# Kernel tuning notes

Measured on AMD Instinct MI355X. Metric: run time of the kernel, lower is better.

## Reference

```python
import jax, jax.numpy as jnp
import numpy as np

N_NODES = 100000
N_EDGES = 1250000
D_FEAT = 64
UNITS = 64


def setup_inputs() -> dict:
    key = jax.random.key(0)
    k1, k2, k3 = jax.random.split(key, 3)
    features = jax.random.normal(k1, (N_NODES, D_FEAT), dtype=jnp.float32)
    edge_index = jax.random.randint(k2, (2, N_EDGES), 0, N_NODES, dtype=jnp.int64)
    weight = jax.random.normal(k3, (D_FEAT, UNITS), dtype=jnp.float32) * (1.0 / np.sqrt(D_FEAT))
    bias = jnp.zeros((UNITS,), dtype=jnp.float32)
    return {"features": features, "edge_index": edge_index, "weight": weight, "bias": bias}


def reference(features, edge_index, weight, bias):
    num_nodes = features.shape[0]
    row = edge_index[0]  # [E] destination rows of adjacency
    col = edge_index[1]  # [E] source columns
    ones = jnp.ones(row.shape[0], dtype=features.dtype)
    # degree_i = number of edges with row == i (sparse row-sum of all-ones adj)
    degrees = jax.ops.segment_sum(ones, row, num_segments=num_nodes)
    deg_inv_sqrt = jnp.power(degrees, -0.5)
    deg_inv_sqrt = jnp.where(jnp.isfinite(deg_inv_sqrt), deg_inv_sqrt, 0.0)
    # symmetric normalization per edge: D^{-1/2} A D^{-1/2}
    w = deg_inv_sqrt[row] * deg_inv_sqrt[col]  # [E]
    # SpMM: propagated[i] = sum_{e: row_e = i} w_e * features[col_e]
    msgs = features[col] * w[:, None]  # [E, F]
    propagated = jax.ops.segment_sum(msgs, row, num_segments=num_nodes)  # [N, F]
    h = propagated @ weight + bias
    return jax.nn.relu(h)
```

## Files before the change

kernel.cpp:

```cpp
#include <hip/hip_runtime.h>
#include <hip/hip_bf16.h>

#define DFEAT 64
#define SBSHIFT 9
#define SBROWS 512
#define CAPSHIFT 13
#define CAP 8192
#define CHUNK 2048

typedef __attribute__((ext_vector_type(8))) unsigned short ushort8;

static __device__ __forceinline__ unsigned short f2bf(float f) {
    __hip_bfloat16 h = __float2bfloat16(f);
    unsigned short u;
    __builtin_memcpy(&u, &h, 2);
    return u;
}

__global__ __launch_bounds__(256) void xw_binA_kernel(
        const float* __restrict__ feat, const float* __restrict__ W,
        ushort8* __restrict__ Y, int n,
        const int* __restrict__ ei, int E,
        int* __restrict__ sbcursor, int* __restrict__ packed, int xwBlocks) {
    __shared__ float4 sW[DFEAT * 16];
    __shared__ int hist[256];
    __shared__ int cur[256];

    if (blockIdx.x < xwBlocks) {
        for (int i = threadIdx.x; i < DFEAT * 16; i += blockDim.x)
            sW[i] = ((const float4*)W)[i];
        __syncthreads();

        int q = threadIdx.x & 3;
        int lrow = threadIdx.x >> 2;
        int lane = threadIdx.x & 63;
        int qbase = lane & ~3;
        int row = blockIdx.x * 64 + lrow;

        float4 x[4];
        if (row < n) {
            const float4* xp = (const float4*)(feat + (size_t)row * DFEAT) + q * 4;
            x[0] = xp[0]; x[1] = xp[1]; x[2] = xp[2]; x[3] = xp[3];
        } else {
            x[0] = x[1] = x[2] = x[3] = make_float4(0.f, 0.f, 0.f, 0.f);
        }

        float4 acc[4];
#pragma unroll
        for (int j = 0; j < 4; j++) acc[j] = make_float4(0.f, 0.f, 0.f, 0.f);

#pragma unroll
        for (int qp = 0; qp < 4; qp++) {
#pragma unroll
            for (int jj = 0; jj < 4; jj++) {
                float xs[4];
                xs[0] = __shfl(x[jj].x, qbase + qp);
                xs[1] = __shfl(x[jj].y, qbase + qp);
                xs[2] = __shfl(x[jj].z, qbase + qp);
                xs[3] = __shfl(x[jj].w, qbase + qp);
                int k0 = qp * 16 + jj * 4;
#pragma unroll
                for (int c = 0; c < 4; c++) {
                    const float4* wrow = &sW[(k0 + c) * 16 + q * 4];
#pragma unroll
                    for (int j = 0; j < 4; j++) {
                        float4 w = wrow[j];
                        acc[j].x = fmaf(xs[c], w.x, acc[j].x);
                        acc[j].y = fmaf(xs[c], w.y, acc[j].y);
                        acc[j].z = fmaf(xs[c], w.z, acc[j].z);
                        acc[j].w = fmaf(xs[c], w.w, acc[j].w);
                    }
                }
            }
        }

        if (row < n) {
            ushort8 o0, o1;
            o0[0] = f2bf(acc[0].x); o0[1] = f2bf(acc[0].y);
            o0[2] = f2bf(acc[0].z); o0[3] = f2bf(acc[0].w);
            o0[4] = f2bf(acc[1].x); o0[5] = f2bf(acc[1].y);
            o0[6] = f2bf(acc[1].z); o0[7] = f2bf(acc[1].w);
            o1[0] = f2bf(acc[2].x); o1[1] = f2bf(acc[2].y);
            o1[2] = f2bf(acc[2].z); o1[3] = f2bf(acc[2].w);
            o1[4] = f2bf(acc[3].x); o1[5] = f2bf(acc[3].y);
            o1[6] = f2bf(acc[3].z); o1[7] = f2bf(acc[3].w);
            ushort8* Yo = Y + (size_t)row * 8 + q * 2;
            Yo[0] = o0;
            Yo[1] = o1;
        }
    } else {
        int bid = blockIdx.x - xwBlocks;
        int t = threadIdx.x;
        hist[t] = 0;
        __syncthreads();
        int base = bid * CHUNK;
        for (int k = 0; k < CHUNK; k += 256) {
            int idx = base + k + t;
            if (idx < E) atomicAdd(&hist[ei[idx] >> SBSHIFT], 1);
        }
        __syncthreads();
        int h = hist[t];
        cur[t] = (h > 0) ? atomicAdd(&sbcursor[t], h) : 0;
        __syncthreads();
        for (int k = 0; k < CHUNK; k += 256) {
            int idx = base + k + t;
            if (idx < E) {
                int r = ei[idx];
                int c = ei[E + idx];
                int sb = r >> SBSHIFT;
                int p = atomicAdd(&cur[sb], 1);
                if (p < CAP)
                    packed[(sb << CAPSHIFT) + p] = ((r & (SBROWS - 1)) << 17) | c;
            }
        }
    }
}

__global__ void binB_kernel(const int* __restrict__ sbcursor, const int* __restrict__ packed,
                            int* __restrict__ csr_col, int* __restrict__ row_beg,
                            int* __restrict__ row_end, float* __restrict__ dis, int n) {
    __shared__ int rcnt[SBROWS];
    __shared__ int rcur[SBROWS];
    int sb = blockIdx.x;
    int t = threadIdx.x;
    int cnt = min(sbcursor[sb], CAP);
    const int* pk = packed + ((size_t)sb << CAPSHIFT);
    for (int i = t; i < SBROWS; i += 256) rcnt[i] = 0;
    __syncthreads();
    for (int i = t; i < cnt; i += 256) atomicAdd(&rcnt[pk[i] >> 17], 1);
    __syncthreads();
    if (t < 64) {
        int v[8];
        int run = 0;
#pragma unroll
        for (int k = 0; k < 8; k++) { v[k] = run; run += rcnt[t * 8 + k]; }
        int x = run;
        for (int off = 1; off < 64; off <<= 1) {
            int y = __shfl_up(x, off);
            if (t >= off) x += y;
        }
        int excl = x - run;
#pragma unroll
        for (int k = 0; k < 8; k++) rcur[t * 8 + k] = excl + v[k];
    }
    __syncthreads();
    int rows = min(SBROWS, n - sb * SBROWS);
    for (int rl = t; rl < rows; rl += 256) {
        int beg = (sb << CAPSHIFT) + rcur[rl];
        int d = rcnt[rl];
        int r = sb * SBROWS + rl;
        row_beg[r] = beg;
        row_end[r] = beg + d;
        dis[r] = (d > 0) ? rsqrtf((float)d) : 0.0f;
    }
    __syncthreads();
    for (int i = t; i < cnt; i += 256) {
        int p = pk[i];
        int pos = atomicAdd(&rcur[p >> 17], 1);
        csr_col[(sb << CAPSHIFT) + pos] = p & 0x1FFFF;
    }
}

__global__ __launch_bounds__(256) void spmm_kernel(
        const int* __restrict__ row_beg, const int* __restrict__ row_end,
        const int* __restrict__ csr_col, const float* __restrict__ dis,
        const ushort8* __restrict__ Y, const float* __restrict__ bias,
        float* __restrict__ out, int n) {
    int wid = (int)(((long long)blockIdx.x * blockDim.x + threadIdx.x) >> 6);
    int lane = threadIdx.x & 63;
    int h = lane >> 5;
    int lane5 = lane & 31;
    int hbase = h << 5;
    int row = wid * 2 + h;
    bool active = row < n;
    int s = active ? row_beg[row] : 0;
    int e = active ? row_end[row] : 0;
    int sub = lane5 >> 3;
    int f8 = lane5 & 7;
    float acc[8] = {0.f, 0.f, 0.f, 0.f, 0.f, 0.f, 0.f, 0.f};
    for (int base = s; base < e; base += 32) {
        int cnt = min(32, e - base);
        int c = 0;
        float dv = 0.f;
        if (lane5 < cnt) { c = csr_col[base + lane5]; dv = dis[c]; }
        for (int i = 0; i < cnt; i += 4) {
            int idx = i + sub;
            int ce = __shfl(c, hbase + idx);
            float de = __shfl(dv, hbase + idx);
            if (idx < cnt) {
                ushort8 y = Y[(size_t)ce * 8 + f8];
#pragma unroll
                for (int k = 0; k < 8; k++)
                    acc[k] = fmaf(de, __uint_as_float(((unsigned)y[k]) << 16), acc[k]);
            }
        }
    }
#pragma unroll
    for (int k = 0; k < 8; k++) {
        acc[k] += __shfl_xor(acc[k], 8);
        acc[k] += __shfl_xor(acc[k], 16);
    }
    if (active && sub == 0) {
        float dr = dis[row];
        float4 b0 = ((const float4*)bias)[f8 * 2];
        float4 b1 = ((const float4*)bias)[f8 * 2 + 1];
        float4 o0, o1;
        o0.x = fmaxf(fmaf(dr, acc[0], b0.x), 0.f);
        o0.y = fmaxf(fmaf(dr, acc[1], b0.y), 0.f);
        o0.z = fmaxf(fmaf(dr, acc[2], b0.z), 0.f);
        o0.w = fmaxf(fmaf(dr, acc[3], b0.w), 0.f);
        o1.x = fmaxf(fmaf(dr, acc[4], b1.x), 0.f);
        o1.y = fmaxf(fmaf(dr, acc[5], b1.y), 0.f);
        o1.z = fmaxf(fmaf(dr, acc[6], b1.z), 0.f);
        o1.w = fmaxf(fmaf(dr, acc[7], b1.w), 0.f);
        float4* op = (float4*)(out + (size_t)row * DFEAT + f8 * 8);
        op[0] = o0;
        op[1] = o1;
    }
}

extern "C" void kernel_launch(void* const* d_in, const int* in_sizes, int n_in,
                              void* d_out, int out_size, void* d_ws, size_t ws_size,
                              hipStream_t stream) {
    const float* feat = (const float*)d_in[0];
    const int*   ei   = (const int*)d_in[1];
    const float* W    = (const float*)d_in[2];
    const float* bias = (const float*)d_in[3];
    float* out = (float*)d_out;

    int n = in_sizes[0] / DFEAT;
    int E = in_sizes[1] / 2;
    int nSB = (n + SBROWS - 1) >> SBSHIFT;

    int* ws = (int*)d_ws;
    size_t o = 0;
    int*   sbcursor = ws + o; o += 256;
    float* dis      = (float*)(ws + o); o += (size_t)n;
    int*   row_beg  = ws + o; o += (size_t)n;
    int*   row_end  = ws + o; o += (size_t)n;
    int*   packed   = ws + o; o += (size_t)nSB << CAPSHIFT;
    int*   csr_col  = ws + o; o += (size_t)nSB << CAPSHIFT;
    ushort8* Y      = (ushort8*)(ws + o);

    hipMemsetAsync(sbcursor, 0, 256 * sizeof(int), stream);

    int xwBlocks = (n + 63) / 64;
    int binABlocks = (E + CHUNK - 1) / CHUNK;
    xw_binA_kernel<<<xwBlocks + binABlocks, 256, 0, stream>>>(
        feat, W, Y, n, ei, E, sbcursor, packed, xwBlocks);
    binB_kernel<<<nSB, 256, 0, stream>>>(sbcursor, packed, csr_col, row_beg, row_end, dis, n);
    spmm_kernel<<<((n + 1) / 2 + 3) / 4, 256, 0, stream>>>(
        row_beg, row_end, csr_col, dis, Y, bias, out, n);
}
```

Before: 167.1 us.

## Stage binned edges in LDS and write contiguous runs per superblock

The binning pass now takes larger chunks per block. It computes a local prefix scan of the per-superblock histogram and scatters edge payloads into shared memory grouped by superblock. Each wave then copies contiguous runs to the global packed buffer, replacing scattered per-edge global writes with coalesced ones. The global cursors are padded to separate cache lines to cut atomic contention. In exchange there are fewer, larger binning blocks, more shared memory per block (lower occupancy for the xw path sharing the kernel), and an extra sync and copy pass.

```diff
diff --git a/kernel.cpp b/kernel.cpp
--- a/kernel.cpp
+++ b/kernel.cpp
@@ -6,7 +6,8 @@
 #define SBROWS 512
 #define CAPSHIFT 13
 #define CAP 8192
-#define CHUNK 2048
+#define CHUNK 8192
+#define CURPAD 16
 
 typedef __attribute__((ext_vector_type(8))) unsigned short ushort8;
 
@@ -22,11 +23,10 @@
         ushort8* __restrict__ Y, int n,
         const int* __restrict__ ei, int E,
         int* __restrict__ sbcursor, int* __restrict__ packed, int xwBlocks) {
-    __shared__ float4 sW[DFEAT * 16];
-    __shared__ int hist[256];
-    __shared__ int cur[256];
+    __shared__ __align__(16) char smem[CHUNK * 4 + 4 * 256 * 4];
 
     if (blockIdx.x < xwBlocks) {
+        float4* sW = (float4*)smem;
         for (int i = threadIdx.x; i < DFEAT * 16; i += blockDim.x)
             sW[i] = ((const float4*)W)[i];
         __syncthreads();
@@ -89,28 +89,67 @@
             Yo[1] = o1;
         }
     } else {
+        int* pay   = (int*)smem;
+        int* hist  = (int*)(smem + CHUNK * 4);
+        int* lbase = hist + 256;
+        int* cur2  = lbase + 256;
+        int* gbase = cur2 + 256;
+
         int bid = blockIdx.x - xwBlocks;
         int t = threadIdx.x;
+        int base = bid * CHUNK;
         hist[t] = 0;
         __syncthreads();
-        int base = bid * CHUNK;
+
         for (int k = 0; k < CHUNK; k += 256) {
             int idx = base + k + t;
             if (idx < E) atomicAdd(&hist[ei[idx] >> SBSHIFT], 1);
         }
         __syncthreads();
+
         int h = hist[t];
-        cur[t] = (h > 0) ? atomicAdd(&sbcursor[t], h) : 0;
-        __syncthreads();
+        gbase[t] = (h > 0) ? atomicAdd(&sbcursor[t * CURPAD], h) : 0;
+        if (t < 64) {
+            int v[4];
+            int run = 0;
+#pragma unroll
+            for (int k = 0; k < 4; k++) { v[k] = run; run += hist[t * 4 + k]; }
+            int x = run;
+            for (int off = 1; off < 64; off <<= 1) {
+                int y = __shfl_up(x, off);
+                if (t >= off) x += y;
+            }
+            int excl = x - run;
+#pragma unroll
+            for (int k = 0; k < 4; k++) {
+                lbase[t * 4 + k] = excl + v[k];
+                cur2[t * 4 + k] = excl + v[k];
+            }
+        }
+        __syncthreads();
+
         for (int k = 0; k < CHUNK; k += 256) {
             int idx = base + k + t;
             if (idx < E) {
                 int r = ei[idx];
                 int c = ei[E + idx];
                 int sb = r >> SBSHIFT;
-                int p = atomicAdd(&cur[sb], 1);
-                if (p < CAP)
-                    packed[(sb << CAPSHIFT) + p] = ((r & (SBROWS - 1)) << 17) | c;
+                int pos = atomicAdd(&cur2[sb], 1);
+                pay[pos] = ((r & (SBROWS - 1)) << 17) | c;
+            }
+        }
+        __syncthreads();
+
+        int wave = t >> 6;
+        int lane = t & 63;
+        for (int sbi = wave; sbi < 256; sbi += 4) {
+            int len = hist[sbi];
+            int lb = lbase[sbi];
+            int gb = gbase[sbi];
+            int* dst = packed + (sbi << CAPSHIFT);
+            for (int i = lane; i < len; i += 64) {
+                int gpos = gb + i;
+                if (gpos < CAP) dst[gpos] = pay[lb + i];
             }
         }
     }
@@ -123,7 +162,7 @@
     __shared__ int rcur[SBROWS];
     int sb = blockIdx.x;
     int t = threadIdx.x;
-    int cnt = min(sbcursor[sb], CAP);
+    int cnt = min(sbcursor[sb * CURPAD], CAP);
     const int* pk = packed + ((size_t)sb << CAPSHIFT);
     for (int i = t; i < SBROWS; i += 256) rcnt[i] = 0;
     __syncthreads();
@@ -234,7 +273,7 @@
 
     int* ws = (int*)d_ws;
     size_t o = 0;
-    int*   sbcursor = ws + o; o += 256;
+    int*   sbcursor = ws + o; o += 256 * CURPAD;
     float* dis      = (float*)(ws + o); o += (size_t)n;
     int*   row_beg  = ws + o; o += (size_t)n;
     int*   row_end  = ws + o; o += (size_t)n;
@@ -242,7 +281,7 @@
     int*   csr_col  = ws + o; o += (size_t)nSB << CAPSHIFT;
     ushort8* Y      = (ushort8*)(ws + o);
 
-    hipMemsetAsync(sbcursor, 0, 256 * sizeof(int), stream);
+    hipMemsetAsync(sbcursor, 0, 256 * CURPAD * sizeof(int), stream);
 
     int xwBlocks = (n + 63) / 64;
     int binABlocks = (E + CHUNK - 1) / CHUNK;
```

New measurement: 176.7 us. +5.8%, slower.

## Schedule binning blocks first, cache row indices in registers, pad global cursors

Applied to the files above, without the earlier changes.

Reorders the fused kernel so the edge-binning blocks get the low block IDs and are dispatched before the feature-transform blocks, starting the longer binning work earlier. Each binning block now handles twice as many edges and keeps the row indices in registers between the histogram pass and the scatter pass, so the row array is read once instead of twice. The global per-superblock cursors are spaced 16 ints apart to reduce contention on shared cache lines, and the two branches share one aliased shared-memory buffer. The trade-offs are more registers per thread and fewer binning blocks to spread the atomic traffic.

```diff
diff --git a/kernel.cpp b/kernel.cpp
--- a/kernel.cpp
+++ b/kernel.cpp
@@ -6,7 +6,9 @@
 #define SBROWS 512
 #define CAPSHIFT 13
 #define CAP 8192
-#define CHUNK 2048
+#define CHUNK 4096
+#define RPT 16
+#define CURPAD 16
 
 typedef __attribute__((ext_vector_type(8))) unsigned short ushort8;
 
@@ -17,25 +19,58 @@
     return u;
 }
 
-__global__ __launch_bounds__(256) void xw_binA_kernel(
+__global__ __launch_bounds__(256) void binA_xw_kernel(
         const float* __restrict__ feat, const float* __restrict__ W,
         ushort8* __restrict__ Y, int n,
         const int* __restrict__ ei, int E,
-        int* __restrict__ sbcursor, int* __restrict__ packed, int xwBlocks) {
-    __shared__ float4 sW[DFEAT * 16];
-    __shared__ int hist[256];
-    __shared__ int cur[256];
-
-    if (blockIdx.x < xwBlocks) {
+        int* __restrict__ sbcursor, int* __restrict__ packed, int binABlocks) {
+    __shared__ __align__(16) char smem[16384];
+
+    if (blockIdx.x < binABlocks) {
+        int* hist = (int*)smem;
+        int* cur  = hist + 256;
+        int t = threadIdx.x;
+        hist[t] = 0;
+        __syncthreads();
+
+        int base = blockIdx.x * CHUNK;
+        int rv[RPT];
+#pragma unroll
+        for (int k = 0; k < RPT; k++) {
+            int idx = base + k * 256 + t;
+            rv[k] = (idx < E) ? ei[idx] : -1;
+            if (rv[k] >= 0) atomicAdd(&hist[rv[k] >> SBSHIFT], 1);
+        }
+        __syncthreads();
+
+        int h = hist[t];
+        cur[t] = (h > 0) ? atomicAdd(&sbcursor[t * CURPAD], h) : 0;
+        __syncthreads();
+
+#pragma unroll
+        for (int k = 0; k < RPT; k++) {
+            int idx = base + k * 256 + t;
+            if (rv[k] >= 0) {
+                int r = rv[k];
+                int c = ei[E + idx];
+                int sb = r >> SBSHIFT;
+                int pos = atomicAdd(&cur[sb], 1);
+                if (pos < CAP)
+                    packed[(sb << CAPSHIFT) + pos] = ((r & (SBROWS - 1)) << 17) | c;
+            }
+        }
+    } else {
+        float4* sW = (float4*)smem;
         for (int i = threadIdx.x; i < DFEAT * 16; i += blockDim.x)
             sW[i] = ((const float4*)W)[i];
         __syncthreads();
 
+        int bid = blockIdx.x - binABlocks;
         int q = threadIdx.x & 3;
         int lrow = threadIdx.x >> 2;
         int lane = threadIdx.x & 63;
         int qbase = lane & ~3;
-        int row = blockIdx.x * 64 + lrow;
+        int row = bid * 64 + lrow;
 
         float4 x[4];
         if (row < n) {
@@ -88,31 +123,6 @@
             Yo[0] = o0;
             Yo[1] = o1;
         }
-    } else {
-        int bid = blockIdx.x - xwBlocks;
-        int t = threadIdx.x;
-        hist[t] = 0;
-        __syncthreads();
-        int base = bid * CHUNK;
-        for (int k = 0; k < CHUNK; k += 256) {
-            int idx = base + k + t;
-            if (idx < E) atomicAdd(&hist[ei[idx] >> SBSHIFT], 1);
-        }
-        __syncthreads();
-        int h = hist[t];
-        cur[t] = (h > 0) ? atomicAdd(&sbcursor[t], h) : 0;
-        __syncthreads();
-        for (int k = 0; k < CHUNK; k += 256) {
-            int idx = base + k + t;
-            if (idx < E) {
-                int r = ei[idx];
-                int c = ei[E + idx];
-                int sb = r >> SBSHIFT;
-                int p = atomicAdd(&cur[sb], 1);
-                if (p < CAP)
-                    packed[(sb << CAPSHIFT) + p] = ((r & (SBROWS - 1)) << 17) | c;
-            }
-        }
     }
 }
 
@@ -123,7 +133,7 @@
     __shared__ int rcur[SBROWS];
     int sb = blockIdx.x;
     int t = threadIdx.x;
-    int cnt = min(sbcursor[sb], CAP);
+    int cnt = min(sbcursor[sb * CURPAD], CAP);
     const int* pk = packed + ((size_t)sb << CAPSHIFT);
     for (int i = t; i < SBROWS; i += 256) rcnt[i] = 0;
     __syncthreads();
@@ -234,7 +244,7 @@
 
     int* ws = (int*)d_ws;
     size_t o = 0;
-    int*   sbcursor = ws + o; o += 256;
+    int*   sbcursor = ws + o; o += 256 * CURPAD;
     float* dis      = (float*)(ws + o); o += (size_t)n;
     int*   row_beg  = ws + o; o += (size_t)n;
     int*   row_end  = ws + o; o += (size_t)n;
@@ -242,12 +252,12 @@
     int*   csr_col  = ws + o; o += (size_t)nSB << CAPSHIFT;
     ushort8* Y      = (ushort8*)(ws + o);
 
-    hipMemsetAsync(sbcursor, 0, 256 * sizeof(int), stream);
-
+    hipMemsetAsync(sbcursor, 0, 256 * CURPAD * sizeof(int), stream);
+
+    int binABlocks = (E + CHUNK - 1) / CHUNK;
     int xwBlocks = (n + 63) / 64;
-    int binABlocks = (E + CHUNK - 1) / CHUNK;
-    xw_binA_kernel<<<xwBlocks + binABlocks, 256, 0, stream>>>(
-        feat, W, Y, n, ei, E, sbcursor, packed, xwBlocks);
+    binA_xw_kernel<<<binABlocks + xwBlocks, 256, 0, stream>>>(
+        feat, W, Y, n, ei, E, sbcursor, packed, binABlocks);
     binB_kernel<<<nSB, 256, 0, stream>>>(sbcursor, packed, csr_col, row_beg, row_end, dis, n);
     spmm_kernel<<<((n + 1) / 2 + 3) / 4, 256, 0, stream>>>(
         row_beg, row_end, csr_col, dis, Y, bias, out, n);
```

New measurement: 160.8 us. -3.8%, faster.
